# Kernel optimization log

Measured on AMD Instinct MI355X. Metric: run time of the kernel, lower is better.

The kernel has to match this reference:

```python
import jax, jax.numpy as jnp
import numpy as np

N_NODES = 100000
N_EDGES = 1600000
NODE_DIM = 32
EDGE_DIM = 16
OUT_DIM = 32


def setup_inputs() -> dict:
    key = jax.random.key(0)
    ks = jax.random.split(key, 8)
    D = NODE_DIM + EDGE_DIM  # 48
    return {
        "y": jax.random.normal(ks[0], (N_NODES, NODE_DIM), dtype=jnp.float32),
        "ex": jax.random.normal(ks[1], (N_EDGES, EDGE_DIM), dtype=jnp.float32),
        "W1": jax.random.normal(ks[2], (D, D), dtype=jnp.float32) / np.sqrt(D),
        "b1": jax.random.normal(ks[3], (D,), dtype=jnp.float32) * 0.01,
        "W2": jax.random.normal(ks[4], (OUT_DIM, D), dtype=jnp.float32) / np.sqrt(D),
        "b2": jax.random.normal(ks[5], (OUT_DIM,), dtype=jnp.float32) * 0.01,
        "src": jax.random.randint(ks[6], (N_EDGES,), 0, N_NODES, dtype=jnp.int32),
        "dst": jax.random.randint(ks[7], (N_EDGES,), 0, N_NODES, dtype=jnp.int32),
    }


def reference(y, ex, W1, b1, W2, b2, src, dst):
    n_nodes = y.shape[0]
    # per-edge message: ReLU(Linear(concat(y[src], e_x)))  -> [E, node_dim+edge_dim]
    feat = jnp.concatenate([y[src], ex], axis=1)
    m = jax.nn.relu(feat @ W1.T + b1)
    # mean scatter-reduce onto destination nodes (0 for isolated nodes, DGL semantics)
    s = jax.ops.segment_sum(m, dst, num_segments=n_nodes)
    cnt = jax.ops.segment_sum(jnp.ones((m.shape[0],), m.dtype), dst, num_segments=n_nodes)
    z = jnp.where(cnt[:, None] > 0, s / jnp.maximum(cnt, 1.0)[:, None], 0.0)
    # node update: ReLU(Linear(z)) -> [N, out_dim]
    h = jax.nn.relu(z @ W2.T + b2)
    return h
```

## Files before the change

kernel.cpp:

```cpp
#include <hip/hip_runtime.h>

#define NODE_DIM 32
#define EDGE_DIM 16
#define DD 48
#define OUT_DIM 32
#define MAXDEG 64
#define STAGED 32
#define NXCD 8
#define NPW 8

typedef _Float16 f16x8 __attribute__((ext_vector_type(8)));
typedef float f32x4 __attribute__((ext_vector_type(4)));

__global__ __launch_bounds__(256)
void prep_scatter_kernel(const int* __restrict__ dst, const int* __restrict__ src,
                         int* __restrict__ cursor, int2* __restrict__ meta,
                         int E, int NP, int K, int G,
                         const float* __restrict__ y, _Float16* __restrict__ yh,
                         int CBy, const float* __restrict__ ex,
                         _Float16* __restrict__ exh, int N) {
    const int b  = blockIdx.x;
    const int g  = b >> 3;
    const int r8 = b & 7;
    const long long gk = (long long)g * K;
    const int s0 = (int)(gk / G);
    const int s1 = (int)((gk + K) / G);

    if (s1 > s0) {
        const int base = s0 * 2048 + threadIdx.x * 8;
        if (base >= E) return;
        int dv[8], sv[8];
        if (base + 8 <= E) {
            *reinterpret_cast<int4*>(dv)     = *reinterpret_cast<const int4*>(dst + base);
            *reinterpret_cast<int4*>(dv + 4) = *reinterpret_cast<const int4*>(dst + base + 4);
            *reinterpret_cast<int4*>(sv)     = *reinterpret_cast<const int4*>(src + base);
            *reinterpret_cast<int4*>(sv + 4) = *reinterpret_cast<const int4*>(src + base + 4);
        } else {
#pragma unroll
            for (int i = 0; i < 8; ++i) {
                dv[i] = (base + i < E) ? dst[base + i] : -1;
                sv[i] = (base + i < E) ? src[base + i] : 0;
            }
        }
#pragma unroll
        for (int i = 0; i < 8; ++i) {
            const int d = dv[i];
            if (d >= 0 && (d & (NXCD - 1)) == r8 && base + i < E) {
                int pos = atomicAdd(&cursor[r8 * NP + (d >> 3)], 1);
                if (pos < MAXDEG)
                    meta[(size_t)d * MAXDEG + pos] = make_int2(base + i, sv[i]);
            }
        }
        return;
    }

    int cb = (g - s0) * 8 + r8;
    if (cb < CBy) {
        size_t i = ((size_t)cb * 256 + threadIdx.x) * 8;
        if (i < (size_t)N * NODE_DIM) {
            const float4* p = reinterpret_cast<const float4*>(y + i);
            const float4 a = p[0], c = p[1];
            f16x8 h = {(_Float16)a.x, (_Float16)a.y, (_Float16)a.z, (_Float16)a.w,
                       (_Float16)c.x, (_Float16)c.y, (_Float16)c.z, (_Float16)c.w};
            *reinterpret_cast<f16x8*>(yh + i) = h;
        }
        return;
    }
    cb -= CBy;
    size_t i = ((size_t)cb * 256 + threadIdx.x) * 8;
    if (i < (size_t)E * EDGE_DIM) {
        const float4* p = reinterpret_cast<const float4*>(ex + i);
        const float4 a = p[0], c = p[1];
        f16x8 h = {(_Float16)a.x, (_Float16)a.y, (_Float16)a.z, (_Float16)a.w,
                   (_Float16)c.x, (_Float16)c.y, (_Float16)c.z, (_Float16)c.w};
        *reinterpret_cast<f16x8*>(exh + i) = h;
    }
}

__global__ __launch_bounds__(256)
void fused_kernel(const _Float16* __restrict__ yh, const _Float16* __restrict__ exh,
                  const float* __restrict__ W1, const float* __restrict__ b1,
                  const float* __restrict__ W2, const float* __restrict__ b2,
                  const int* __restrict__ cursor, const int2* __restrict__ meta,
                  float* __restrict__ out, int N, int NP) {
    __shared__ int2 mlds[4][NPW][STAGED];
    __shared__ _Float16 zl[4][NPW][64];

    const int wave = threadIdx.x >> 6;
    const int lane = threadIdx.x & 63;
    const int col = lane & 15;
    const int kg  = lane >> 4;

    f16x8 Blo[3], Bhi[3];
#pragma unroll
    for (int t = 0; t < 3; ++t) {
        const float* wr = W1 + (size_t)(t * 16 + col) * DD;
#pragma unroll
        for (int j = 0; j < 8; ++j) {
            Blo[t][j] = (_Float16)wr[kg * 8 + j];
            Bhi[t][j] = (_Float16)0.f;
        }
        if (kg < 2) {
#pragma unroll
            for (int j = 0; j < 8; ++j)
                Bhi[t][j] = (_Float16)wr[NODE_DIM + kg * 8 + j];
        }
        if (kg == 3) Bhi[t][7] = (_Float16)b1[t * 16 + col];
    }

    const int nb0 = (blockIdx.x * 4 + wave) * NPW;

    int dgv = 0;
    if (lane < NPW) {
        const int n = nb0 + lane;
        if (n < N) dgv = cursor[(n & (NXCD - 1)) * NP + (n >> 3)];
    }

#pragma unroll
    for (int ni = 0; ni < NPW; ++ni) {
        const int cnt_i = min(__shfl(dgv, ni), STAGED);
        const int n = nb0 + ni;
        if (lane < STAGED)
            mlds[wave][ni][lane] = (lane < cnt_i && n < N)
                                       ? meta[(size_t)n * MAXDEG + lane]
                                       : make_int2(0, 0);
    }
    __builtin_amdgcn_wave_barrier();

    for (int ni = 0; ni < NPW; ++ni) {
        const int n = nb0 + ni;
        const int dg = __shfl(dgv, ni);
        const int cnt = min(dg, MAXDEG);

        float pacc0 = 0.f, pacc1 = 0.f, pacc2 = 0.f;
        const int ngroups = (cnt + 15) >> 4;

        for (int g = 0; g < ngroups; ++g) {
            const int row = g * 16 + col;
            const bool valid = row < cnt;
            const int2 md = (row < STAGED)
                                ? mlds[wave][ni][row]
                                : (valid ? meta[(size_t)n * MAXDEG + row]
                                         : make_int2(0, 0));
            const int eid = md.x, sv = md.y;

            f16x8 alo = *reinterpret_cast<const f16x8*>(
                yh + (size_t)sv * NODE_DIM + kg * 8);

            f16x8 ahi;
            if (kg < 2) {
                ahi = *reinterpret_cast<const f16x8*>(
                    exh + (size_t)eid * EDGE_DIM + kg * 8);
            } else {
#pragma unroll
                for (int j = 0; j < 8; ++j) ahi[j] = (_Float16)0.f;
                if (kg == 3) ahi[7] = (_Float16)1.f;
            }

            if (!valid) {
#pragma unroll
                for (int j = 0; j < 8; ++j) { alo[j] = (_Float16)0.f; ahi[j] = (_Float16)0.f; }
            }

#pragma unroll
            for (int t = 0; t < 3; ++t) {
                f32x4 c = {0.f, 0.f, 0.f, 0.f};
                c = __builtin_amdgcn_mfma_f32_16x16x32_f16(alo, Blo[t], c, 0, 0, 0);
                c = __builtin_amdgcn_mfma_f32_16x16x32_f16(ahi, Bhi[t], c, 0, 0, 0);
#pragma unroll
                for (int r = 0; r < 4; ++r) {
                    const float v = fmaxf(c[r], 0.f);
                    if (t == 0) pacc0 += v;
                    else if (t == 1) pacc1 += v;
                    else pacc2 += v;
                }
            }
        }

        pacc0 += __shfl_xor(pacc0, 16); pacc0 += __shfl_xor(pacc0, 32);
        pacc1 += __shfl_xor(pacc1, 16); pacc1 += __shfl_xor(pacc1, 32);
        pacc2 += __shfl_xor(pacc2, 16); pacc2 += __shfl_xor(pacc2, 32);

        if (n < N) {
            const float inv = (dg > 0) ? 1.f / (float)dg : 0.f;
            if (lane < 16) {
                zl[wave][ni][lane]      = (_Float16)(pacc0 * inv);
                zl[wave][ni][lane + 16] = (_Float16)(pacc1 * inv);
                zl[wave][ni][lane + 32] = (_Float16)(pacc2 * inv);
            }
            if (lane < 8) {
                const unsigned int v = (lane == 0) ? 0x00003C00u : 0u;
                *reinterpret_cast<unsigned int*>(&zl[wave][ni][48 + lane * 2]) = v;
            }
        } else if (lane < 32) {
            *reinterpret_cast<unsigned int*>(&zl[wave][ni][lane * 2]) = 0u;
        }
    }

    f16x8 Wf[2][2];
#pragma unroll
    for (int t = 0; t < 2; ++t) {
#pragma unroll
        for (int c = 0; c < 2; ++c) {
            f16x8 v;
#pragma unroll
            for (int j = 0; j < 8; ++j) {
                const int k = c * 32 + kg * 8 + j;
                float w = 0.f;
                if (k < DD)       w = W2[(size_t)(t * 16 + col) * DD + k];
                else if (k == DD) w = b2[t * 16 + col];
                v[j] = (_Float16)w;
            }
            Wf[t][c] = v;
        }
    }

    __builtin_amdgcn_wave_barrier();
    const _Float16* zr = &zl[wave][col & (NPW - 1)][0];
    const f16x8 A0 = *reinterpret_cast<const f16x8*>(zr + kg * 8);
    const f16x8 A1 = *reinterpret_cast<const f16x8*>(zr + 32 + kg * 8);

#pragma unroll
    for (int t = 0; t < 2; ++t) {
        f32x4 h = {0.f, 0.f, 0.f, 0.f};
        h = __builtin_amdgcn_mfma_f32_16x16x32_f16(A0, Wf[t][0], h, 0, 0, 0);
        h = __builtin_amdgcn_mfma_f32_16x16x32_f16(A1, Wf[t][1], h, 0, 0, 0);
#pragma unroll
        for (int r = 0; r < 4; ++r) {
            const int mrow = kg * 4 + r;
            const int node = nb0 + mrow;
            if (mrow < NPW && node < N)
                out[(size_t)node * OUT_DIM + t * 16 + col] = fmaxf(h[r], 0.f);
        }
    }
}

extern "C" void kernel_launch(void* const* d_in, const int* in_sizes, int n_in,
                              void* d_out, int out_size, void* d_ws, size_t ws_size,
                              hipStream_t stream) {
    const float* y  = (const float*)d_in[0];
    const float* ex = (const float*)d_in[1];
    const float* W1 = (const float*)d_in[2];
    const float* b1 = (const float*)d_in[3];
    const float* W2 = (const float*)d_in[4];
    const float* b2 = (const float*)d_in[5];
    const int* src  = (const int*)d_in[6];
    const int* dst  = (const int*)d_in[7];

    const int N = in_sizes[0] / NODE_DIM;
    const int E = in_sizes[6];
    const int NP = (N + NXCD - 1) / NXCD;
    const int NC = ((NXCD * NP + 3) / 4) * 4;

    int* cursor = (int*)d_ws;
    size_t off  = ((size_t)NC * sizeof(int) + 255) & ~(size_t)255;
    int2* meta  = (int2*)((char*)d_ws + off);
    _Float16* yh = (_Float16*)((char*)meta + (size_t)N * MAXDEG * sizeof(int2));
    _Float16* exh = (_Float16*)((char*)yh + (size_t)N * NODE_DIM * sizeof(_Float16));

    const int CBy = (N * NODE_DIM / 8 + 255) / 256;
    const int CBe = (E * EDGE_DIM / 8 + 255) / 256;
    const int K   = (E + 2047) / 2048;
    const int CG  = (CBy + CBe + 7) / 8;
    const int G   = K + CG;

    hipMemsetAsync(cursor, 0, (size_t)NC * sizeof(int), stream);

    prep_scatter_kernel<<<G * 8, 256, 0, stream>>>(dst, src, cursor, meta,
                                                   E, NP, K, G,
                                                   y, yh, CBy, ex, exh, N);

    const int NB = (N + NPW * 4 - 1) / (NPW * 4);
    fused_kernel<<<NB, 256, 0, stream>>>(yh, exh, W1, b1, W2, b2,
                                         cursor, meta, (float*)d_out, N, NP);
}
```

Baseline: 173.7 us.

## Software-pipeline edge gathers across fixed 16-edge groups with prefetch

Flattens the per-node, variable-length group loop into a fixed, fully unrolled sequence of two 16-edge groups per node. The gather loads for the next group are issued before the MFMAs for the current group, and any edges beyond the staged 32 go through a separate tail loop. This is meant to hide gather latency behind the MFMA work. In exchange, every node now costs two groups even when its degree is small, the unrolled code uses more registers, and launch bounds now request 8 blocks per CU, which could force spills.

```diff
diff --git a/kernel.cpp b/kernel.cpp
--- a/kernel.cpp
+++ b/kernel.cpp
@@ -77,7 +77,7 @@
     }
 }
 
-__global__ __launch_bounds__(256)
+__global__ __launch_bounds__(256, 8)
 void fused_kernel(const _Float16* __restrict__ yh, const _Float16* __restrict__ exh,
                   const float* __restrict__ W1, const float* __restrict__ b1,
                   const float* __restrict__ W2, const float* __restrict__ b2,
@@ -127,74 +127,119 @@
     }
     __builtin_amdgcn_wave_barrier();
 
-    for (int ni = 0; ni < NPW; ++ni) {
-        const int n = nb0 + ni;
+    f16x8 ahiC;
+#pragma unroll
+    for (int j = 0; j < 8; ++j) ahiC[j] = (_Float16)0.f;
+    if (kg == 3) ahiC[7] = (_Float16)1.f;
+
+    float pacc0 = 0.f, pacc1 = 0.f, pacc2 = 0.f;
+
+    f16x8 cA, cB, nA, nB;
+    {
+        const int2 md = mlds[wave][0][col];
+        cA = *reinterpret_cast<const f16x8*>(yh + (size_t)md.y * NODE_DIM + kg * 8);
+        cB = ahiC;
+        if (kg < 2)
+            cB = *reinterpret_cast<const f16x8*>(exh + (size_t)md.x * EDGE_DIM + kg * 8);
+    }
+
+#pragma unroll
+    for (int k = 0; k < 2 * NPW; ++k) {
+        const int ni = k >> 1;
+        const int g  = k & 1;
+
+        if (k < 2 * NPW - 1) {
+            const int ni2 = (k + 1) >> 1;
+            const int g2  = (k + 1) & 1;
+            const int2 md = mlds[wave][ni2][g2 * 16 + col];
+            nA = *reinterpret_cast<const f16x8*>(yh + (size_t)md.y * NODE_DIM + kg * 8);
+            nB = ahiC;
+            if (kg < 2)
+                nB = *reinterpret_cast<const f16x8*>(exh + (size_t)md.x * EDGE_DIM + kg * 8);
+        }
+
         const int dg = __shfl(dgv, ni);
         const int cnt = min(dg, MAXDEG);
-
-        float pacc0 = 0.f, pacc1 = 0.f, pacc2 = 0.f;
-        const int ngroups = (cnt + 15) >> 4;
-
-        for (int g = 0; g < ngroups; ++g) {
-            const int row = g * 16 + col;
-            const bool valid = row < cnt;
-            const int2 md = (row < STAGED)
-                                ? mlds[wave][ni][row]
-                                : (valid ? meta[(size_t)n * MAXDEG + row]
-                                         : make_int2(0, 0));
-            const int eid = md.x, sv = md.y;
-
-            f16x8 alo = *reinterpret_cast<const f16x8*>(
-                yh + (size_t)sv * NODE_DIM + kg * 8);
-
-            f16x8 ahi;
-            if (kg < 2) {
-                ahi = *reinterpret_cast<const f16x8*>(
-                    exh + (size_t)eid * EDGE_DIM + kg * 8);
-            } else {
-#pragma unroll
-                for (int j = 0; j < 8; ++j) ahi[j] = (_Float16)0.f;
-                if (kg == 3) ahi[7] = (_Float16)1.f;
-            }
-
-            if (!valid) {
-#pragma unroll
-                for (int j = 0; j < 8; ++j) { alo[j] = (_Float16)0.f; ahi[j] = (_Float16)0.f; }
-            }
-
-#pragma unroll
-            for (int t = 0; t < 3; ++t) {
-                f32x4 c = {0.f, 0.f, 0.f, 0.f};
-                c = __builtin_amdgcn_mfma_f32_16x16x32_f16(alo, Blo[t], c, 0, 0, 0);
-                c = __builtin_amdgcn_mfma_f32_16x16x32_f16(ahi, Bhi[t], c, 0, 0, 0);
-#pragma unroll
-                for (int r = 0; r < 4; ++r) {
-                    const float v = fmaxf(c[r], 0.f);
-                    if (t == 0) pacc0 += v;
-                    else if (t == 1) pacc1 += v;
-                    else pacc2 += v;
+        const bool valid = (g * 16 + col) < cnt;
+
+        f16x8 a = cA, bb = cB;
+        if (!valid) {
+#pragma unroll
+            for (int j = 0; j < 8; ++j) { a[j] = (_Float16)0.f; bb[j] = (_Float16)0.f; }
+        }
+
+#pragma unroll
+        for (int t = 0; t < 3; ++t) {
+            f32x4 c = {0.f, 0.f, 0.f, 0.f};
+            c = __builtin_amdgcn_mfma_f32_16x16x32_f16(a,  Blo[t], c, 0, 0, 0);
+            c = __builtin_amdgcn_mfma_f32_16x16x32_f16(bb, Bhi[t], c, 0, 0, 0);
+#pragma unroll
+            for (int r = 0; r < 4; ++r) {
+                const float v = fmaxf(c[r], 0.f);
+                if (t == 0) pacc0 += v;
+                else if (t == 1) pacc1 += v;
+                else pacc2 += v;
+            }
+        }
+
+        if (g == 1) {
+            const int n = nb0 + ni;
+
+            if (cnt > STAGED) {
+                const int ngroups = (cnt + 15) >> 4;
+                for (int gg = 2; gg < ngroups; ++gg) {
+                    const int row = gg * 16 + col;
+                    const bool v2 = row < cnt;
+                    const int2 md = v2 ? meta[(size_t)n * MAXDEG + row]
+                                       : make_int2(0, 0);
+                    f16x8 ta = *reinterpret_cast<const f16x8*>(
+                        yh + (size_t)md.y * NODE_DIM + kg * 8);
+                    f16x8 tb = ahiC;
+                    if (kg < 2)
+                        tb = *reinterpret_cast<const f16x8*>(
+                            exh + (size_t)md.x * EDGE_DIM + kg * 8);
+                    if (!v2) {
+#pragma unroll
+                        for (int j = 0; j < 8; ++j) { ta[j] = (_Float16)0.f; tb[j] = (_Float16)0.f; }
+                    }
+#pragma unroll
+                    for (int t = 0; t < 3; ++t) {
+                        f32x4 c = {0.f, 0.f, 0.f, 0.f};
+                        c = __builtin_amdgcn_mfma_f32_16x16x32_f16(ta, Blo[t], c, 0, 0, 0);
+                        c = __builtin_amdgcn_mfma_f32_16x16x32_f16(tb, Bhi[t], c, 0, 0, 0);
+#pragma unroll
+                        for (int r = 0; r < 4; ++r) {
+                            const float v = fmaxf(c[r], 0.f);
+                            if (t == 0) pacc0 += v;
+                            else if (t == 1) pacc1 += v;
+                            else pacc2 += v;
+                        }
+                    }
                 }
             }
-        }
-
-        pacc0 += __shfl_xor(pacc0, 16); pacc0 += __shfl_xor(pacc0, 32);
-        pacc1 += __shfl_xor(pacc1, 16); pacc1 += __shfl_xor(pacc1, 32);
-        pacc2 += __shfl_xor(pacc2, 16); pacc2 += __shfl_xor(pacc2, 32);
-
-        if (n < N) {
-            const float inv = (dg > 0) ? 1.f / (float)dg : 0.f;
-            if (lane < 16) {
-                zl[wave][ni][lane]      = (_Float16)(pacc0 * inv);
-                zl[wave][ni][lane + 16] = (_Float16)(pacc1 * inv);
-                zl[wave][ni][lane + 32] = (_Float16)(pacc2 * inv);
-            }
-            if (lane < 8) {
-                const unsigned int v = (lane == 0) ? 0x00003C00u : 0u;
-                *reinterpret_cast<unsigned int*>(&zl[wave][ni][48 + lane * 2]) = v;
-            }
-        } else if (lane < 32) {
-            *reinterpret_cast<unsigned int*>(&zl[wave][ni][lane * 2]) = 0u;
-        }
+
+            pacc0 += __shfl_xor(pacc0, 16); pacc0 += __shfl_xor(pacc0, 32);
+            pacc1 += __shfl_xor(pacc1, 16); pacc1 += __shfl_xor(pacc1, 32);
+            pacc2 += __shfl_xor(pacc2, 16); pacc2 += __shfl_xor(pacc2, 32);
+
+            if (n < N) {
+                const float inv = (dg > 0) ? 1.f / (float)dg : 0.f;
+                if (lane < 16) {
+                    zl[wave][ni][lane]      = (_Float16)(pacc0 * inv);
+                    zl[wave][ni][lane + 16] = (_Float16)(pacc1 * inv);
+                    zl[wave][ni][lane + 32] = (_Float16)(pacc2 * inv);
+                }
+                if (lane < 8) {
+                    const unsigned int v = (lane == 0) ? 0x00003C00u : 0u;
+                    *reinterpret_cast<unsigned int*>(&zl[wave][ni][48 + lane * 2]) = v;
+                }
+            } else if (lane < 32) {
+                *reinterpret_cast<unsigned int*>(&zl[wave][ni][lane * 2]) = 0u;
+            }
+            pacc0 = 0.f; pacc1 = 0.f; pacc2 = 0.f;
+        }
+
+        cA = nA; cB = nB;
     }
 
     f16x8 Wf[2][2];
```

Result: slower. 296.6 us (+70.7%).
